# Kernel optimization log

Measured on AMD Instinct MI355X. Metric: run time of the kernel, lower is better.

The kernel has to match this reference:

```python
import jax, jax.numpy as jnp
import numpy as np

B, S, H, F, E, K = 2, 2048, 1024, 4096, 8, 2


def setup_inputs() -> dict:
    key = jax.random.key(0)
    ks = jax.random.split(key, 6)
    x = jax.random.normal(ks[0], (B, S, H), dtype=jnp.float32)
    probs = jax.random.uniform(ks[1], (K, B, S, 1), dtype=jnp.float32)
    experts = jax.random.randint(ks[2], (K, B, S, 1), 0, E, dtype=jnp.int32)
    # per-expert FFN params; 0.02 scale mimics typical transformer init
    w1 = jax.random.normal(ks[3], (E, H, F), dtype=jnp.float32) * 0.02
    b1 = jnp.zeros((E, F), dtype=jnp.float32)
    w2 = jax.random.normal(ks[4], (E, F, H), dtype=jnp.float32) * 0.02
    b2 = jnp.zeros((E, H), dtype=jnp.float32)
    return {"x": x, "probs": probs, "experts": experts,
            "w1": w1, "b1": b1, "w2": w2, "b2": b2}


def reference(x, probs, experts, w1, b1, w2, b2):
    # Dense compute-all-experts FFN: every expert processes every token.
    h = jnp.einsum('bsh,ehf->ebsf', x, w1) + b1[:, None, None, :]  # [E,B,S,F]
    h = jax.nn.gelu(h)
    y = jnp.einsum('ebsf,efh->ebsh', h, w2) + b2[:, None, None, :]  # [E,B,S,H]
    # Masked combine: sum_e sum_j probs_j * y_e * (experts_j == e)
    onehot = jax.nn.one_hot(experts[..., 0], w1.shape[0], dtype=x.dtype)  # [K,B,S,E]
    weights = jnp.einsum('kbsl,kbse->bse', probs, onehot)  # [B,S,E]
    out = jnp.einsum('bse,ebsh->bsh', weights, y)
    return out
```

## Files before the change

kernel.cpp:

```cpp
#include <hip/hip_runtime.h>
#include <stdint.h>

#define H_DIM 1024
#define F_DIM 4096
#define E_NUM 8
#define T_NUM 4096
#define NE    8192
#define BM    128
#define BN    128
#define BK    64
#define MAXTILES 72
#define PADMAX (MAXTILES*BM)

#define M_NT  0
#define M_PB  1
#define M_CNT 16
#define M_CUR 24
#define M_TE  32
#define M_TR  104
#define M_INTS 176

typedef float  f32x4  __attribute__((ext_vector_type(4)));
typedef short  bf16x8 __attribute__((ext_vector_type(8)));
typedef __bf16 b16v8  __attribute__((ext_vector_type(8)));
typedef unsigned short u16;
typedef u16    u16x8  __attribute__((ext_vector_type(8)));

__device__ __forceinline__ float gelu_tanh(float v) {
  float u = 0.7978845608028654f * (v + 0.044715f * v * v * v);
  return v / (1.0f + __expf(-2.0f * u));
}

__device__ __forceinline__ float b2f(u16 v) {
  union { float f; unsigned u; } x; x.u = ((unsigned)v) << 16; return x.f;
}

__device__ __forceinline__ void gl16(const void* g, void* l) {
  __builtin_amdgcn_global_load_lds(
      (const __attribute__((address_space(1))) unsigned int*)g,
      (__attribute__((address_space(3))) unsigned int*)l, 16, 0, 0);
}


__global__ void k_init(int* tok, float* wgt, int* meta) {
  int i = blockIdx.x * 256 + threadIdx.x;
  if (i < PADMAX) { tok[i] = 0; wgt[i] = 0.f; }
  if (i < E_NUM) { meta[M_CNT + i] = 0; meta[M_CUR + i] = 0; }
}

__global__ void k_count(const int* __restrict__ experts, int* meta) {
  int i = blockIdx.x * 256 + threadIdx.x;
  int e = experts[i];
  int lane = threadIdx.x & 63;
#pragma unroll
  for (int ee = 0; ee < E_NUM; ++ee) {
    unsigned long long bm = __ballot(e == ee);
    if (e == ee && lane == __builtin_ctzll(bm))
      atomicAdd(&meta[M_CNT + ee], __popcll(bm));
  }
}

__global__ void k_plan(int* meta) {
  if (threadIdx.x != 0 || blockIdx.x != 0) return;
  int pb = 0, idx = 0;
  for (int e = 0; e < E_NUM; ++e) {
    int c = meta[M_CNT + e];
    int nt = (c + BM - 1) / BM;
    meta[M_PB + e] = pb;
    for (int t = 0; t < nt; ++t) { meta[M_TE + idx] = e; meta[M_TR + idx] = pb + t * BM; ++idx; }
    pb += nt * BM;
  }
  meta[M_NT] = idx;
}

__global__ void k_scatter(const int* __restrict__ experts, const float* __restrict__ probs,
                          int* tok, float* wgt, int* entpos, int* meta) {
  int i = blockIdx.x * 256 + threadIdx.x;
  int e = experts[i];
  int t = i & (T_NUM - 1);
  float p = probs[i];
  int lane = threadIdx.x & 63;
#pragma unroll
  for (int ee = 0; ee < E_NUM; ++ee) {
    unsigned long long bm = __ballot(e == ee);
    if (e == ee) {
      int leader = __builtin_ctzll(bm);
      int cnt = __popcll(bm);
      int base = 0;
      if (lane == leader) base = atomicAdd(&meta[M_CUR + ee], cnt);
      base = __shfl(base, leader);
      int rank = __popcll(bm & ((1ull << lane) - 1ull));
      int pos = meta[M_PB + ee] + base + rank;
      tok[pos] = t;
      wgt[pos] = p;
      entpos[i] = pos;
    }
  }
}

__global__ void k_cvt_x(const float* __restrict__ x, u16* __restrict__ xbf) {
  int i = blockIdx.x * 256 + threadIdx.x;
  const f32x4* xp = (const f32x4*)x;
  f32x4 a = xp[i * 2], b = xp[i * 2 + 1];
  b16v8 o;
  o[0] = (__bf16)a[0]; o[1] = (__bf16)a[1]; o[2] = (__bf16)a[2]; o[3] = (__bf16)a[3];
  o[4] = (__bf16)b[0]; o[5] = (__bf16)b[1]; o[6] = (__bf16)b[2]; o[7] = (__bf16)b[3];
  ((b16v8*)xbf)[i] = o;
}

__global__ __launch_bounds__(256) void k_trans(const float* __restrict__ W, u16* __restrict__ Wt,
                                               int R, int C) {
  alignas(16) __shared__ char L[16384];
  int e = blockIdx.z;
  int r0 = blockIdx.y * 64, c0 = blockIdx.x * 64;
  const float* We = W + (size_t)e * R * C;
  u16* Wte = Wt + (size_t)e * R * C;
  int tid = threadIdx.x;
#pragma unroll
  for (int it = 0; it < 4; ++it) {
    int gi = it * 256 + tid;
    int row = gi >> 4, c4 = gi & 15;
    f32x4 v = *(const f32x4*)(We + (size_t)(r0 + row) * C + c0 + c4 * 4);
    *(f32x4*)(L + row * 256 + ((c4 ^ (row & 15)) * 16)) = v;
  }
  __syncthreads();
#pragma unroll
  for (int s = 0; s < 2; ++s) {
    int chunk = s * 256 + tid;
    int c = chunk >> 3, rb = chunk & 7;
    b16v8 o;
#pragma unroll
    for (int j = 0; j < 8; ++j) {
      int r = rb * 8 + j;
      float f = *(const float*)(L + r * 256 + (((c >> 2) ^ (r & 15)) * 16) + (c & 3) * 4);
      o[j] = (__bf16)f;
    }
    *(b16v8*)(void*)(Wte + (size_t)(c0 + c) * R + r0 + rb * 8) = o;
  }
}


__global__ __launch_bounds__(256) void k_gemm1(
    const u16* __restrict__ xbf, const u16* __restrict__ w1t, const float* __restrict__ b1,
    const int* __restrict__ tok, const int* __restrict__ meta, u16* __restrict__ hbuf)
{
  int nt = meta[M_NT];
  int slot = blockIdx.x;
  if (slot >= nt) return;
  int e     = meta[M_TE + slot];
  int rbase = meta[M_TR + slot];
  int cbase = blockIdx.y * BN;

  alignas(16) __shared__ char LDS[32768];
  char* Alds = LDS;
  char* Blds = LDS + 16384;

  int tid = threadIdx.x;
  int lane = tid & 63;
  int wid = tid >> 6;
  int wr = wid >> 1, wc = wid & 1;
  int ks = lane & 7, r8 = lane >> 3;

  const u16* asrc[4]; const u16* bsrc[4]; char* adst[4]; char* bdst[4];
#pragma unroll
  for (int j = 0; j < 4; ++j) {
    int r = wid * 32 + j * 8 + r8;
    int t = tok[rbase + r];
    asrc[j] = xbf + (size_t)t * H_DIM + ((ks ^ (r & 7)) * 8);
    bsrc[j] = w1t + ((size_t)e * F_DIM + cbase + r) * H_DIM + ((ks ^ (r & 7)) * 8);
    adst[j] = Alds + (wid * 32 + j * 8) * 128;
    bdst[j] = Blds + (wid * 32 + j * 8) * 128;
  }

  f32x4 acc[4][4];
#pragma unroll
  for (int m = 0; m < 4; ++m)
#pragma unroll
    for (int n = 0; n < 4; ++n) acc[m][n] = (f32x4){0.f, 0.f, 0.f, 0.f};

  for (int kt = 0; kt < H_DIM / BK; ++kt) {
    int kb = kt * BK;
    if (kt) __syncthreads();
#pragma unroll
    for (int j = 0; j < 4; ++j) gl16(asrc[j] + kb, adst[j]);
#pragma unroll
    for (int j = 0; j < 4; ++j) gl16(bsrc[j] + kb, bdst[j]);
    __syncthreads();
#pragma unroll
    for (int kk = 0; kk < 2; ++kk) {
      int kbyte = kk * 64 + ((lane >> 4) << 4);
      bf16x8 af[4], bfr[4];
#pragma unroll
      for (int m = 0; m < 4; ++m) {
        int r = wr * 64 + m * 16 + (lane & 15);
        af[m] = *(const bf16x8*)(Alds + r * 128 + (kbyte ^ ((r & 7) << 4)));
      }
#pragma unroll
      for (int n = 0; n < 4; ++n) {
        int c = wc * 64 + n * 16 + (lane & 15);
        bfr[n] = *(const bf16x8*)(Blds + c * 128 + (kbyte ^ ((c & 7) << 4)));
      }
#pragma unroll
      for (int m = 0; m < 4; ++m)
#pragma unroll
        for (int n = 0; n < 4; ++n)
          acc[m][n] = __builtin_amdgcn_mfma_f32_16x16x32_bf16(af[m], bfr[n], acc[m][n], 0, 0, 0);
    }
  }

  __syncthreads();
  float bv[4];
#pragma unroll
  for (int n = 0; n < 4; ++n) bv[n] = b1[e * F_DIM + cbase + wc * 64 + n * 16 + (lane & 15)];
  char* reg = LDS + wid * 8192;
#pragma unroll
  for (int m = 0; m < 4; ++m)
#pragma unroll
    for (int n = 0; n < 4; ++n)
#pragma unroll
      for (int q = 0; q < 4; ++q) {
        float v = acc[m][n][q] + bv[n];
        v = gelu_tanh(v);
        int row4 = ((lane >> 4) << 2) + q;
        int col = n * 16 + (lane & 15);
        *(__bf16*)(reg + m * 2048 + row4 * 128 + col * 2) = (__bf16)v;
      }
  __syncthreads();
#pragma unroll
  for (int q = 0; q < 8; ++q) {
    int m = q >> 1, p = q & 1;
    int byte = p * 1024 + lane * 16;
    u16x8 v = *(const u16x8*)(reg + m * 2048 + byte);
    int row  = p * 8 + (lane >> 3);
    int colb = (lane & 7) * 16;
    size_t grow = (size_t)(rbase + wr * 64 + m * 16 + row);
    size_t gcol = (size_t)(cbase + wc * 64 + (colb >> 1));
    *(u16x8*)(hbuf + grow * F_DIM + gcol) = v;
  }
}


__global__ __launch_bounds__(256) void k_gemm2(
    const u16* __restrict__ hbuf, const u16* __restrict__ w2t, const float* __restrict__ b2,
    const int* __restrict__ meta, u16* __restrict__ ybuf)
{
  int nt = meta[M_NT];
  int slot = blockIdx.x;
  if (slot >= nt) return;
  int e     = meta[M_TE + slot];
  int rbase = meta[M_TR + slot];
  int cbase = blockIdx.y * BN;
  int kzb   = blockIdx.z * (F_DIM / 2);

  alignas(16) __shared__ char LDS[32768];
  char* Alds = LDS;
  char* Blds = LDS + 16384;

  int tid = threadIdx.x;
  int lane = tid & 63;
  int wid = tid >> 6;
  int wr = wid >> 1, wc = wid & 1;
  int ks = lane & 7, r8 = lane >> 3;

  const u16* asrc[4]; const u16* bsrc[4]; char* adst[4]; char* bdst[4];
#pragma unroll
  for (int j = 0; j < 4; ++j) {
    int r = wid * 32 + j * 8 + r8;
    asrc[j] = hbuf + (size_t)(rbase + r) * F_DIM + kzb + ((ks ^ (r & 7)) * 8);
    bsrc[j] = w2t + ((size_t)e * H_DIM + cbase + r) * F_DIM + kzb + ((ks ^ (r & 7)) * 8);
    adst[j] = Alds + (wid * 32 + j * 8) * 128;
    bdst[j] = Blds + (wid * 32 + j * 8) * 128;
  }

  f32x4 acc[4][4];
#pragma unroll
  for (int m = 0; m < 4; ++m)
#pragma unroll
    for (int n = 0; n < 4; ++n) acc[m][n] = (f32x4){0.f, 0.f, 0.f, 0.f};

  for (int kt = 0; kt < (F_DIM / 2) / BK; ++kt) {
    int kb = kt * BK;
    if (kt) __syncthreads();
#pragma unroll
    for (int j = 0; j < 4; ++j) gl16(asrc[j] + kb, adst[j]);
#pragma unroll
    for (int j = 0; j < 4; ++j) gl16(bsrc[j] + kb, bdst[j]);
    __syncthreads();
#pragma unroll
    for (int kk = 0; kk < 2; ++kk) {
      int kbyte = kk * 64 + ((lane >> 4) << 4);
      bf16x8 af[4], bfr[4];
#pragma unroll
      for (int m = 0; m < 4; ++m) {
        int r = wr * 64 + m * 16 + (lane & 15);
        af[m] = *(const bf16x8*)(Alds + r * 128 + (kbyte ^ ((r & 7) << 4)));
      }
#pragma unroll
      for (int n = 0; n < 4; ++n) {
        int c = wc * 64 + n * 16 + (lane & 15);
        bfr[n] = *(const bf16x8*)(Blds + c * 128 + (kbyte ^ ((c & 7) << 4)));
      }
#pragma unroll
      for (int m = 0; m < 4; ++m)
#pragma unroll
        for (int n = 0; n < 4; ++n)
          acc[m][n] = __builtin_amdgcn_mfma_f32_16x16x32_bf16(af[m], bfr[n], acc[m][n], 0, 0, 0);
    }
  }

  __syncthreads();
  bool z0 = (blockIdx.z == 0);
  u16* yb = ybuf + (size_t)blockIdx.z * PADMAX * H_DIM;
  float bv[4];
#pragma unroll
  for (int n = 0; n < 4; ++n)
    bv[n] = z0 ? b2[e * H_DIM + cbase + wc * 64 + n * 16 + (lane & 15)] : 0.f;
  char* reg = LDS + wid * 8192;
#pragma unroll
  for (int m = 0; m < 4; ++m)
#pragma unroll
    for (int n = 0; n < 4; ++n)
#pragma unroll
      for (int q = 0; q < 4; ++q) {
        float v = acc[m][n][q] + bv[n];
        int row4 = ((lane >> 4) << 2) + q;
        int col = n * 16 + (lane & 15);
        *(__bf16*)(reg + m * 2048 + row4 * 128 + col * 2) = (__bf16)v;
      }
  __syncthreads();
#pragma unroll
  for (int q = 0; q < 8; ++q) {
    int m = q >> 1, p = q & 1;
    int byte = p * 1024 + lane * 16;
    u16x8 v = *(const u16x8*)(reg + m * 2048 + byte);
    int row  = p * 8 + (lane >> 3);
    int colb = (lane & 7) * 16;
    size_t grow = (size_t)(rbase + wr * 64 + m * 16 + row);
    size_t gcol = (size_t)(cbase + wc * 64 + (colb >> 1));
    *(u16x8*)(yb + grow * H_DIM + gcol) = v;
  }
}


__global__ __launch_bounds__(256) void k_combine(
    const u16* __restrict__ ybuf, const float* __restrict__ wgt,
    const int* __restrict__ entpos, float* __restrict__ out)
{
  int idx = blockIdx.x * 256 + threadIdx.x;
  int t = idx >> 7, hc = idx & 127;
  int p0 = entpos[t], p1 = entpos[T_NUM + t];
  float w0 = wgt[p0], w1 = wgt[p1];
  const u16x8* y0 = (const u16x8*)(ybuf);
  const u16x8* y1 = (const u16x8*)(ybuf + (size_t)PADMAX * H_DIM);
  u16x8 a = y0[(size_t)p0 * (H_DIM / 8) + hc];
  u16x8 b = y1[(size_t)p0 * (H_DIM / 8) + hc];
  u16x8 c = y0[(size_t)p1 * (H_DIM / 8) + hc];
  u16x8 d = y1[(size_t)p1 * (H_DIM / 8) + hc];
  f32x4 o0, o1;
#pragma unroll
  for (int j = 0; j < 4; ++j)
    o0[j] = w0 * (b2f(a[j]) + b2f(b[j])) + w1 * (b2f(c[j]) + b2f(d[j]));
#pragma unroll
  for (int j = 0; j < 4; ++j)
    o1[j] = w0 * (b2f(a[4 + j]) + b2f(b[4 + j])) + w1 * (b2f(c[4 + j]) + b2f(d[4 + j]));
  f32x4* op = (f32x4*)(out + (size_t)t * H_DIM + hc * 8);
  op[0] = o0;
  op[1] = o1;
}


extern "C" void kernel_launch(void* const* d_in, const int* in_sizes, int n_in,
                              void* d_out, int out_size, void* d_ws, size_t ws_size,
                              hipStream_t stream)
{
  const float* x       = (const float*)d_in[0];
  const float* probs   = (const float*)d_in[1];
  const int*   experts = (const int*)d_in[2];
  const float* w1      = (const float*)d_in[3];
  const float* b1      = (const float*)d_in[4];
  const float* w2      = (const float*)d_in[5];
  const float* b2      = (const float*)d_in[6];
  float* out = (float*)d_out;

  char* ws = (char*)d_ws;
  size_t off = 0;
  u16*   hbuf = (u16*)(ws + off);  off += (size_t)PADMAX * F_DIM * sizeof(u16);
  u16*   xbf  = (u16*)(ws + off);  off += (size_t)T_NUM * H_DIM * sizeof(u16);
  u16*   w1t  = (u16*)(ws + off);  off += (size_t)E_NUM * F_DIM * H_DIM * sizeof(u16);
  u16*   w2t  = (u16*)(ws + off);  off += (size_t)E_NUM * F_DIM * H_DIM * sizeof(u16);
  int*   tok  = (int*)(ws + off);  off += (size_t)PADMAX * sizeof(int);
  float* wgt  = (float*)(ws + off); off += (size_t)PADMAX * sizeof(float);
  int*   entpos = (int*)(ws + off); off += (size_t)NE * sizeof(int);
  int*   meta = (int*)(ws + off);  off += M_INTS * sizeof(int);
  u16*   ybuf = w1t;
  (void)ws_size; (void)in_sizes; (void)n_in;

  k_init   <<<dim3((PADMAX + 255) / 256), 256, 0, stream>>>(tok, wgt, meta);
  k_count  <<<dim3(NE / 256), 256, 0, stream>>>(experts, meta);
  k_plan   <<<1, 1, 0, stream>>>(meta);
  k_scatter<<<dim3(NE / 256), 256, 0, stream>>>(experts, probs, tok, wgt, entpos, meta);
  k_cvt_x  <<<dim3(T_NUM * H_DIM / 8 / 256), 256, 0, stream>>>(x, xbf);
  k_trans  <<<dim3(F_DIM / 64, H_DIM / 64, E_NUM), 256, 0, stream>>>(w1, w1t, H_DIM, F_DIM);
  k_trans  <<<dim3(H_DIM / 64, F_DIM / 64, E_NUM), 256, 0, stream>>>(w2, w2t, F_DIM, H_DIM);
  k_gemm1  <<<dim3(MAXTILES, F_DIM / BN), 256, 0, stream>>>(xbf, w1t, b1, tok, meta, hbuf);
  k_gemm2  <<<dim3(MAXTILES, H_DIM / BN, 2), 256, 0, stream>>>(hbuf, w2t, b2, meta, ybuf);
  k_combine<<<dim3(T_NUM * H_DIM / 8 / 256), 256, 0, stream>>>(ybuf, wgt, entpos, out);
}
```

Measured before the change: 358.7 us.

## Use 256-row tiles with triple-buffered async LDS pipeline in expert GEMMs

Both expert GEMM kernels move from a single-buffered 128x128 tile with 256 threads to a 256x128 tile with 512 threads. They use a three-stage ring of LDS buffers filled by global_load_lds, with explicit vmcnt waits and raw barriers so loads of later K-steps overlap MFMA work. MFMA sections get raised wave priority. The two transposed weight buffers now share one workspace region, so the w2 transpose runs after GEMM1, and ybuf gets its own allocation. The aim is to hide global-load latency and halve weight re-reads per token, at the cost of 144 KB of dynamic LDS (limiting occupancy), more padding waste per expert, and a hard tile cap of 39 that could drop tiles in extreme routing distributions.

```diff
diff --git a/kernel.cpp b/kernel.cpp
--- a/kernel.cpp
+++ b/kernel.cpp
@@ -6,25 +6,30 @@
 #define E_NUM 8
 #define T_NUM 4096
 #define NE    8192
-#define BM    128
+#define BM    256
 #define BN    128
 #define BK    64
-#define MAXTILES 72
-#define PADMAX (MAXTILES*BM)
+#define MAXT  39
+#define PADMAX (MAXT*BM)
+#define TILE_BYTES 49152
+#define LDS_BYTES  147456
 
 #define M_NT  0
 #define M_PB  1
 #define M_CNT 16
 #define M_CUR 24
 #define M_TE  32
-#define M_TR  104
-#define M_INTS 176
+#define M_TR  80
+#define M_INTS 128
 
 typedef float  f32x4  __attribute__((ext_vector_type(4)));
 typedef short  bf16x8 __attribute__((ext_vector_type(8)));
 typedef __bf16 b16v8  __attribute__((ext_vector_type(8)));
 typedef unsigned short u16;
 typedef u16    u16x8  __attribute__((ext_vector_type(8)));
+
+#define FENCE() asm volatile("" ::: "memory")
+#define BAR()   __builtin_amdgcn_s_barrier()
 
 __device__ __forceinline__ float gelu_tanh(float v) {
   float u = 0.7978845608028654f * (v + 0.044715f * v * v * v);
@@ -67,7 +72,9 @@
     int c = meta[M_CNT + e];
     int nt = (c + BM - 1) / BM;
     meta[M_PB + e] = pb;
-    for (int t = 0; t < nt; ++t) { meta[M_TE + idx] = e; meta[M_TR + idx] = pb + t * BM; ++idx; }
+    for (int t = 0; t < nt && idx < MAXT; ++t) {
+      meta[M_TE + idx] = e; meta[M_TR + idx] = pb + t * BM; ++idx;
+    }
     pb += nt * BM;
   }
   meta[M_NT] = idx;
@@ -140,10 +147,61 @@
 }
 
 
-__global__ __launch_bounds__(256) void k_gemm1(
-    const u16* __restrict__ xbf, const u16* __restrict__ w1t, const float* __restrict__ b1,
+#define STAGE6(kt, bb)                                                      \
+  { char* Ab_ = LDS + (bb);                                                 \
+    _Pragma("unroll")                                                       \
+    for (int j = 0; j < 4; ++j) gl16(asrc[j] + (kt) * 64, Ab_ + adst[j]);   \
+    _Pragma("unroll")                                                       \
+    for (int j = 0; j < 2; ++j) gl16(bsrc[j] + (kt) * 64, Ab_ + 32768 + bdst[j]); }
+
+#define GEMM_COMPUTE(bb)                                                    \
+  { const char* Ab_ = LDS + (bb); const char* Bb_ = Ab_ + 32768;            \
+    _Pragma("unroll")                                                       \
+    for (int kk = 0; kk < 2; ++kk) {                                        \
+      int kbyte = kk * 64 + ((lane >> 4) << 4);                             \
+      bf16x8 af[4], bfr[4];                                                 \
+      _Pragma("unroll")                                                     \
+      for (int m = 0; m < 4; ++m) {                                         \
+        int r = wr * 64 + m * 16 + (lane & 15);                             \
+        af[m] = *(const bf16x8*)(Ab_ + r * 128 + (kbyte ^ ((r & 7) << 4))); \
+      }                                                                     \
+      _Pragma("unroll")                                                     \
+      for (int n = 0; n < 4; ++n) {                                         \
+        int c = wc * 64 + n * 16 + (lane & 15);                             \
+        bfr[n] = *(const bf16x8*)(Bb_ + c * 128 + (kbyte ^ ((c & 7) << 4)));\
+      }                                                                     \
+      __builtin_amdgcn_s_setprio(1);                                        \
+      _Pragma("unroll")                                                     \
+      for (int m = 0; m < 4; ++m)                                           \
+        _Pragma("unroll")                                                   \
+        for (int n = 0; n < 4; ++n)                                         \
+          acc[m][n] = __builtin_amdgcn_mfma_f32_16x16x32_bf16(af[m], bfr[n], acc[m][n], 0, 0, 0); \
+      __builtin_amdgcn_s_setprio(0);                                        \
+    } }
+
+#define GEMM_KLOOP(NT)                                                      \
+  STAGE6(0, 0); STAGE6(1, TILE_BYTES);                                      \
+  { int bcur = 0, bnext = 2 * TILE_BYTES;                                   \
+    for (int t = 0; t < (NT); ++t) {                                        \
+      FENCE();                                                              \
+      if (t + 2 < (NT)) { STAGE6(t + 2, bnext);                             \
+        asm volatile("s_waitcnt vmcnt(12)" ::: "memory"); }                 \
+      else if (t + 1 < (NT)) { asm volatile("s_waitcnt vmcnt(6)" ::: "memory"); } \
+      else { asm volatile("s_waitcnt vmcnt(0)" ::: "memory"); }             \
+      BAR(); FENCE();                                                       \
+      GEMM_COMPUTE(bcur);                                                   \
+      FENCE(); BAR();                                                       \
+      bcur  = (bcur  == 2 * TILE_BYTES) ? 0 : bcur  + TILE_BYTES;           \
+      bnext = (bnext == 2 * TILE_BYTES) ? 0 : bnext + TILE_BYTES;           \
+    } }                                                                     \
+  FENCE();
+
+
+__global__ __launch_bounds__(512, 2) void k_gemm1(
+    const u16* __restrict__ xbf, const u16* __restrict__ wbuf, const float* __restrict__ b1,
     const int* __restrict__ tok, const int* __restrict__ meta, u16* __restrict__ hbuf)
 {
+  extern __shared__ char LDS[];
   int nt = meta[M_NT];
   int slot = blockIdx.x;
   if (slot >= nt) return;
@@ -151,25 +209,26 @@
   int rbase = meta[M_TR + slot];
   int cbase = blockIdx.y * BN;
 
-  alignas(16) __shared__ char LDS[32768];
-  char* Alds = LDS;
-  char* Blds = LDS + 16384;
-
   int tid = threadIdx.x;
   int lane = tid & 63;
   int wid = tid >> 6;
   int wr = wid >> 1, wc = wid & 1;
-  int ks = lane & 7, r8 = lane >> 3;
-
-  const u16* asrc[4]; const u16* bsrc[4]; char* adst[4]; char* bdst[4];
+  int cc = tid & 7, rr = tid >> 3;
+
+  const u16* asrc[4]; int adst[4];
 #pragma unroll
   for (int j = 0; j < 4; ++j) {
-    int r = wid * 32 + j * 8 + r8;
-    int t = tok[rbase + r];
-    asrc[j] = xbf + (size_t)t * H_DIM + ((ks ^ (r & 7)) * 8);
-    bsrc[j] = w1t + ((size_t)e * F_DIM + cbase + r) * H_DIM + ((ks ^ (r & 7)) * 8);
-    adst[j] = Alds + (wid * 32 + j * 8) * 128;
-    bdst[j] = Blds + (wid * 32 + j * 8) * 128;
+    int rj = j * 64 + rr;
+    int t = tok[rbase + rj];
+    asrc[j] = xbf + (size_t)t * H_DIM + ((cc ^ (rj & 7)) * 8);
+    adst[j] = (j * 64 + wid * 8) * 128;
+  }
+  const u16* bsrc[2]; int bdst[2];
+#pragma unroll
+  for (int j = 0; j < 2; ++j) {
+    int nj = j * 64 + rr;
+    bsrc[j] = wbuf + ((size_t)e * F_DIM + cbase + nj) * H_DIM + ((cc ^ (nj & 7)) * 8);
+    bdst[j] = (j * 64 + wid * 8) * 128;
   }
 
   f32x4 acc[4][4];
@@ -178,37 +237,8 @@
 #pragma unroll
     for (int n = 0; n < 4; ++n) acc[m][n] = (f32x4){0.f, 0.f, 0.f, 0.f};
 
-  for (int kt = 0; kt < H_DIM / BK; ++kt) {
-    int kb = kt * BK;
-    if (kt) __syncthreads();
-#pragma unroll
-    for (int j = 0; j < 4; ++j) gl16(asrc[j] + kb, adst[j]);
-#pragma unroll
-    for (int j = 0; j < 4; ++j) gl16(bsrc[j] + kb, bdst[j]);
-    __syncthreads();
-#pragma unroll
-    for (int kk = 0; kk < 2; ++kk) {
-      int kbyte = kk * 64 + ((lane >> 4) << 4);
-      bf16x8 af[4], bfr[4];
-#pragma unroll
-      for (int m = 0; m < 4; ++m) {
-        int r = wr * 64 + m * 16 + (lane & 15);
-        af[m] = *(const bf16x8*)(Alds + r * 128 + (kbyte ^ ((r & 7) << 4)));
-      }
-#pragma unroll
-      for (int n = 0; n < 4; ++n) {
-        int c = wc * 64 + n * 16 + (lane & 15);
-        bfr[n] = *(const bf16x8*)(Blds + c * 128 + (kbyte ^ ((c & 7) << 4)));
-      }
-#pragma unroll
-      for (int m = 0; m < 4; ++m)
-#pragma unroll
-        for (int n = 0; n < 4; ++n)
-          acc[m][n] = __builtin_amdgcn_mfma_f32_16x16x32_bf16(af[m], bfr[n], acc[m][n], 0, 0, 0);
-    }
-  }
-
-  __syncthreads();
+  GEMM_KLOOP(H_DIM / BK)
+
   float bv[4];
 #pragma unroll
   for (int n = 0; n < 4; ++n) bv[n] = b1[e * F_DIM + cbase + wc * 64 + n * 16 + (lane & 15)];
@@ -225,7 +255,6 @@
         int col = n * 16 + (lane & 15);
         *(__bf16*)(reg + m * 2048 + row4 * 128 + col * 2) = (__bf16)v;
       }
-  __syncthreads();
 #pragma unroll
   for (int q = 0; q < 8; ++q) {
     int m = q >> 1, p = q & 1;
@@ -240,10 +269,11 @@
 }
 
 
-__global__ __launch_bounds__(256) void k_gemm2(
-    const u16* __restrict__ hbuf, const u16* __restrict__ w2t, const float* __restrict__ b2,
+__global__ __launch_bounds__(512, 2) void k_gemm2(
+    const u16* __restrict__ hbuf, const u16* __restrict__ wbuf, const float* __restrict__ b2,
     const int* __restrict__ meta, u16* __restrict__ ybuf)
 {
+  extern __shared__ char LDS[];
   int nt = meta[M_NT];
   int slot = blockIdx.x;
   if (slot >= nt) return;
@@ -252,24 +282,25 @@
   int cbase = blockIdx.y * BN;
   int kzb   = blockIdx.z * (F_DIM / 2);
 
-  alignas(16) __shared__ char LDS[32768];
-  char* Alds = LDS;
-  char* Blds = LDS + 16384;
-
   int tid = threadIdx.x;
   int lane = tid & 63;
   int wid = tid >> 6;
   int wr = wid >> 1, wc = wid & 1;
-  int ks = lane & 7, r8 = lane >> 3;
-
-  const u16* asrc[4]; const u16* bsrc[4]; char* adst[4]; char* bdst[4];
+  int cc = tid & 7, rr = tid >> 3;
+
+  const u16* asrc[4]; int adst[4];
 #pragma unroll
   for (int j = 0; j < 4; ++j) {
-    int r = wid * 32 + j * 8 + r8;
-    asrc[j] = hbuf + (size_t)(rbase + r) * F_DIM + kzb + ((ks ^ (r & 7)) * 8);
-    bsrc[j] = w2t + ((size_t)e * H_DIM + cbase + r) * F_DIM + kzb + ((ks ^ (r & 7)) * 8);
-    adst[j] = Alds + (wid * 32 + j * 8) * 128;
-    bdst[j] = Blds + (wid * 32 + j * 8) * 128;
+    int rj = j * 64 + rr;
+    asrc[j] = hbuf + (size_t)(rbase + rj) * F_DIM + kzb + ((cc ^ (rj & 7)) * 8);
+    adst[j] = (j * 64 + wid * 8) * 128;
+  }
+  const u16* bsrc[2]; int bdst[2];
+#pragma unroll
+  for (int j = 0; j < 2; ++j) {
+    int nj = j * 64 + rr;
+    bsrc[j] = wbuf + ((size_t)e * H_DIM + cbase + nj) * F_DIM + kzb + ((cc ^ (nj & 7)) * 8);
+    bdst[j] = (j * 64 + wid * 8) * 128;
   }
 
   f32x4 acc[4][4];
@@ -278,37 +309,8 @@
 #pragma unroll
     for (int n = 0; n < 4; ++n) acc[m][n] = (f32x4){0.f, 0.f, 0.f, 0.f};
 
-  for (int kt = 0; kt < (F_DIM / 2) / BK; ++kt) {
-    int kb = kt * BK;
-    if (kt) __syncthreads();
-#pragma unroll
-    for (int j = 0; j < 4; ++j) gl16(asrc[j] + kb, adst[j]);
-#pragma unroll
-    for (int j = 0; j < 4; ++j) gl16(bsrc[j] + kb, bdst[j]);
-    __syncthreads();
-#pragma unroll
-    for (int kk = 0; kk < 2; ++kk) {
-      int kbyte = kk * 64 + ((lane >> 4) << 4);
-      bf16x8 af[4], bfr[4];
-#pragma unroll
-      for (int m = 0; m < 4; ++m) {
-        int r = wr * 64 + m * 16 + (lane & 15);
-        af[m] = *(const bf16x8*)(Alds + r * 128 + (kbyte ^ ((r & 7) << 4)));
-      }
-#pragma unroll
-      for (int n = 0; n < 4; ++n) {
-        int c = wc * 64 + n * 16 + (lane & 15);
-        bfr[n] = *(const bf16x8*)(Blds + c * 128 + (kbyte ^ ((c & 7) << 4)));
-      }
-#pragma unroll
-      for (int m = 0; m < 4; ++m)
-#pragma unroll
-        for (int n = 0; n < 4; ++n)
-          acc[m][n] = __builtin_amdgcn_mfma_f32_16x16x32_bf16(af[m], bfr[n], acc[m][n], 0, 0, 0);
-    }
-  }
-
-  __syncthreads();
+  GEMM_KLOOP((F_DIM / 2) / BK)
+
   bool z0 = (blockIdx.z == 0);
   u16* yb = ybuf + (size_t)blockIdx.z * PADMAX * H_DIM;
   float bv[4];
@@ -327,7 +329,6 @@
         int col = n * 16 + (lane & 15);
         *(__bf16*)(reg + m * 2048 + row4 * 128 + col * 2) = (__bf16)v;
       }
-  __syncthreads();
 #pragma unroll
   for (int q = 0; q < 8; ++q) {
     int m = q >> 1, p = q & 1;
@@ -386,23 +387,27 @@
   size_t off = 0;
   u16*   hbuf = (u16*)(ws + off);  off += (size_t)PADMAX * F_DIM * sizeof(u16);
   u16*   xbf  = (u16*)(ws + off);  off += (size_t)T_NUM * H_DIM * sizeof(u16);
-  u16*   w1t  = (u16*)(ws + off);  off += (size_t)E_NUM * F_DIM * H_DIM * sizeof(u16);
-  u16*   w2t  = (u16*)(ws + off);  off += (size_t)E_NUM * F_DIM * H_DIM * sizeof(u16);
+  u16*   wbuf = (u16*)(ws + off);  off += (size_t)E_NUM * F_DIM * H_DIM * sizeof(u16);
+  u16*   ybuf = (u16*)(ws + off);  off += (size_t)2 * PADMAX * H_DIM * sizeof(u16);
   int*   tok  = (int*)(ws + off);  off += (size_t)PADMAX * sizeof(int);
   float* wgt  = (float*)(ws + off); off += (size_t)PADMAX * sizeof(float);
   int*   entpos = (int*)(ws + off); off += (size_t)NE * sizeof(int);
   int*   meta = (int*)(ws + off);  off += M_INTS * sizeof(int);
-  u16*   ybuf = w1t;
   (void)ws_size; (void)in_sizes; (void)n_in;
 
-  k_init   <<<dim3((PADMAX + 255) / 256), 256, 0, stream>>>(tok, wgt, meta);
+  hipFuncSetAttribute(reinterpret_cast<const void*>(&k_gemm1),
+                      hipFuncAttributeMaxDynamicSharedMemorySize, LDS_BYTES);
+  hipFuncSetAttribute(reinterpret_cast<const void*>(&k_gemm2),
+                      hipFuncAttributeMaxDynamicSharedMemorySize, LDS_BYTES);
+
+  k_init   <<<dim3(PADMAX / 256), 256, 0, stream>>>(tok, wgt, meta);
   k_count  <<<dim3(NE / 256), 256, 0, stream>>>(experts, meta);
   k_plan   <<<1, 1, 0, stream>>>(meta);
   k_scatter<<<dim3(NE / 256), 256, 0, stream>>>(experts, probs, tok, wgt, entpos, meta);
   k_cvt_x  <<<dim3(T_NUM * H_DIM / 8 / 256), 256, 0, stream>>>(x, xbf);
-  k_trans  <<<dim3(F_DIM / 64, H_DIM / 64, E_NUM), 256, 0, stream>>>(w1, w1t, H_DIM, F_DIM);
-  k_trans  <<<dim3(H_DIM / 64, F_DIM / 64, E_NUM), 256, 0, stream>>>(w2, w2t, F_DIM, H_DIM);
-  k_gemm1  <<<dim3(MAXTILES, F_DIM / BN), 256, 0, stream>>>(xbf, w1t, b1, tok, meta, hbuf);
-  k_gemm2  <<<dim3(MAXTILES, H_DIM / BN, 2), 256, 0, stream>>>(hbuf, w2t, b2, meta, ybuf);
+  k_trans  <<<dim3(F_DIM / 64, H_DIM / 64, E_NUM), 256, 0, stream>>>(w1, wbuf, H_DIM, F_DIM);
+  k_gemm1  <<<dim3(MAXT, F_DIM / BN), 512, LDS_BYTES, stream>>>(xbf, wbuf, b1, tok, meta, hbuf);
+  k_trans  <<<dim3(H_DIM / 64, F_DIM / 64, E_NUM), 256, 0, stream>>>(w2, wbuf, F_DIM, H_DIM);
+  k_gemm2  <<<dim3(MAXT, H_DIM / BN, 2), 512, LDS_BYTES, stream>>>(hbuf, wbuf, b2, meta, ybuf);
   k_combine<<<dim3(T_NUM * H_DIM / 8 / 256), 256, 0, stream>>>(ybuf, wgt, entpos, out);
 }
```

Result: slower. 408.0 us (+13.7%).

## Double-buffer GEMM K-loop with async LDS loads and XCD-aware tile remap

Applied to the files above, without the earlier changes.

Both expert GEMMs now use two LDS buffers, loading the next K tile while MFMAs run on the current one. This removes the load-then-barrier stall of the single-buffered loop. The grid is flattened to 1D, and block ids are remapped so consecutive work lands on the same XCD (the 8-way interleave), which should improve L2 reuse. MFMA sections also raise wave priority. In exchange, LDS use doubles to 64KB of dynamic shared memory, which may cut occupancy. The removed barrier before the epilogue store relies on each wave only reading its own LDS region.

```diff
diff --git a/kernel.cpp b/kernel.cpp
--- a/kernel.cpp
+++ b/kernel.cpp
@@ -11,6 +11,7 @@
 #define BK    64
 #define MAXTILES 72
 #define PADMAX (MAXTILES*BM)
+#define BUFB  32768
 
 #define M_NT  0
 #define M_PB  1
@@ -25,6 +26,8 @@
 typedef __bf16 b16v8  __attribute__((ext_vector_type(8)));
 typedef unsigned short u16;
 typedef u16    u16x8  __attribute__((ext_vector_type(8)));
+
+#define BAR() __builtin_amdgcn_s_barrier()
 
 __device__ __forceinline__ float gelu_tanh(float v) {
   float u = 0.7978845608028654f * (v + 0.044715f * v * v * v);
@@ -140,20 +143,65 @@
 }
 
 
+#define STAGE8(kt, bb)                                                        \
+  { char* L_ = LDS + (bb);                                                    \
+    _Pragma("unroll")                                                         \
+    for (int j = 0; j < 4; ++j) gl16(asrc[j] + (size_t)(kt) * BK, L_ + aoff[j]); \
+    _Pragma("unroll")                                                         \
+    for (int j = 0; j < 4; ++j) gl16(bsrc[j] + (size_t)(kt) * BK, L_ + 16384 + aoff[j]); }
+
+#define GEMM_COMPUTE(bb)                                                      \
+  { const char* Ab_ = LDS + (bb); const char* Bb_ = LDS + (bb) + 16384;       \
+    _Pragma("unroll")                                                         \
+    for (int kk = 0; kk < 2; ++kk) {                                          \
+      int kbyte = kk * 64 + ((lane >> 4) << 4);                               \
+      bf16x8 af[4], bfr[4];                                                   \
+      _Pragma("unroll")                                                       \
+      for (int m = 0; m < 4; ++m) {                                           \
+        int r = wr * 64 + m * 16 + (lane & 15);                               \
+        af[m] = *(const bf16x8*)(Ab_ + r * 128 + (kbyte ^ ((r & 7) << 4)));   \
+      }                                                                       \
+      _Pragma("unroll")                                                       \
+      for (int n = 0; n < 4; ++n) {                                           \
+        int c = wc * 64 + n * 16 + (lane & 15);                               \
+        bfr[n] = *(const bf16x8*)(Bb_ + c * 128 + (kbyte ^ ((c & 7) << 4)));  \
+      }                                                                       \
+      __builtin_amdgcn_s_setprio(1);                                          \
+      _Pragma("unroll")                                                       \
+      for (int m = 0; m < 4; ++m)                                             \
+        _Pragma("unroll")                                                     \
+        for (int n = 0; n < 4; ++n)                                           \
+          acc[m][n] = __builtin_amdgcn_mfma_f32_16x16x32_bf16(af[m], bfr[n], acc[m][n], 0, 0, 0); \
+      __builtin_amdgcn_s_setprio(0);                                          \
+    } }
+
+#define GEMM_KLOOP(NT)                                                        \
+  STAGE8(0, 0);                                                               \
+  asm volatile("s_waitcnt vmcnt(0)" ::: "memory");                            \
+  BAR();                                                                      \
+  { int cur = 0;                                                              \
+    for (int kt = 0; kt < (NT); ++kt) {                                       \
+      if (kt + 1 < (NT)) STAGE8(kt + 1, (cur ^ 1) * BUFB);                    \
+      GEMM_COMPUTE(cur * BUFB);                                               \
+      asm volatile("s_waitcnt vmcnt(0)" ::: "memory");                        \
+      BAR();                                                                  \
+      cur ^= 1;                                                               \
+    } }
+
+
 __global__ __launch_bounds__(256) void k_gemm1(
     const u16* __restrict__ xbf, const u16* __restrict__ w1t, const float* __restrict__ b1,
     const int* __restrict__ tok, const int* __restrict__ meta, u16* __restrict__ hbuf)
 {
+  extern __shared__ char LDS[];
+  int wg = blockIdx.x;
+  int work = (wg & 7) * 288 + (wg >> 3);
+  int slot = work % MAXTILES;
+  int cbase = (work / MAXTILES) * BN;
   int nt = meta[M_NT];
-  int slot = blockIdx.x;
   if (slot >= nt) return;
   int e     = meta[M_TE + slot];
   int rbase = meta[M_TR + slot];
-  int cbase = blockIdx.y * BN;
-
-  alignas(16) __shared__ char LDS[32768];
-  char* Alds = LDS;
-  char* Blds = LDS + 16384;
 
   int tid = threadIdx.x;
   int lane = tid & 63;
@@ -161,15 +209,14 @@
   int wr = wid >> 1, wc = wid & 1;
   int ks = lane & 7, r8 = lane >> 3;
 
-  const u16* asrc[4]; const u16* bsrc[4]; char* adst[4]; char* bdst[4];
+  const u16* asrc[4]; const u16* bsrc[4]; int aoff[4];
 #pragma unroll
   for (int j = 0; j < 4; ++j) {
     int r = wid * 32 + j * 8 + r8;
     int t = tok[rbase + r];
     asrc[j] = xbf + (size_t)t * H_DIM + ((ks ^ (r & 7)) * 8);
     bsrc[j] = w1t + ((size_t)e * F_DIM + cbase + r) * H_DIM + ((ks ^ (r & 7)) * 8);
-    adst[j] = Alds + (wid * 32 + j * 8) * 128;
-    bdst[j] = Blds + (wid * 32 + j * 8) * 128;
+    aoff[j] = (wid * 32 + j * 8) * 128;
   }
 
   f32x4 acc[4][4];
@@ -178,37 +225,8 @@
 #pragma unroll
     for (int n = 0; n < 4; ++n) acc[m][n] = (f32x4){0.f, 0.f, 0.f, 0.f};
 
-  for (int kt = 0; kt < H_DIM / BK; ++kt) {
-    int kb = kt * BK;
-    if (kt) __syncthreads();
-#pragma unroll
-    for (int j = 0; j < 4; ++j) gl16(asrc[j] + kb, adst[j]);
-#pragma unroll
-    for (int j = 0; j < 4; ++j) gl16(bsrc[j] + kb, bdst[j]);
-    __syncthreads();
-#pragma unroll
-    for (int kk = 0; kk < 2; ++kk) {
-      int kbyte = kk * 64 + ((lane >> 4) << 4);
-      bf16x8 af[4], bfr[4];
-#pragma unroll
-      for (int m = 0; m < 4; ++m) {
-        int r = wr * 64 + m * 16 + (lane & 15);
-        af[m] = *(const bf16x8*)(Alds + r * 128 + (kbyte ^ ((r & 7) << 4)));
-      }
-#pragma unroll
-      for (int n = 0; n < 4; ++n) {
-        int c = wc * 64 + n * 16 + (lane & 15);
-        bfr[n] = *(const bf16x8*)(Blds + c * 128 + (kbyte ^ ((c & 7) << 4)));
-      }
-#pragma unroll
-      for (int m = 0; m < 4; ++m)
-#pragma unroll
-        for (int n = 0; n < 4; ++n)
-          acc[m][n] = __builtin_amdgcn_mfma_f32_16x16x32_bf16(af[m], bfr[n], acc[m][n], 0, 0, 0);
-    }
-  }
-
-  __syncthreads();
+  GEMM_KLOOP(H_DIM / BK)
+
   float bv[4];
 #pragma unroll
   for (int n = 0; n < 4; ++n) bv[n] = b1[e * F_DIM + cbase + wc * 64 + n * 16 + (lane & 15)];
@@ -225,7 +243,6 @@
         int col = n * 16 + (lane & 15);
         *(__bf16*)(reg + m * 2048 + row4 * 128 + col * 2) = (__bf16)v;
       }
-  __syncthreads();
 #pragma unroll
   for (int q = 0; q < 8; ++q) {
     int m = q >> 1, p = q & 1;
@@ -244,17 +261,18 @@
     const u16* __restrict__ hbuf, const u16* __restrict__ w2t, const float* __restrict__ b2,
     const int* __restrict__ meta, u16* __restrict__ ybuf)
 {
+  extern __shared__ char LDS[];
+  int wg = blockIdx.x;
+  int work = (wg & 7) * 144 + (wg >> 3);
+  int zi   = work / 576;
+  int rem  = work % 576;
+  int slot = rem % MAXTILES;
+  int cbase = (rem / MAXTILES) * BN;
+  int kzb   = zi * (F_DIM / 2);
   int nt = meta[M_NT];
-  int slot = blockIdx.x;
   if (slot >= nt) return;
   int e     = meta[M_TE + slot];
   int rbase = meta[M_TR + slot];
-  int cbase = blockIdx.y * BN;
-  int kzb   = blockIdx.z * (F_DIM / 2);
-
-  alignas(16) __shared__ char LDS[32768];
-  char* Alds = LDS;
-  char* Blds = LDS + 16384;
 
   int tid = threadIdx.x;
   int lane = tid & 63;
@@ -262,14 +280,13 @@
   int wr = wid >> 1, wc = wid & 1;
   int ks = lane & 7, r8 = lane >> 3;
 
-  const u16* asrc[4]; const u16* bsrc[4]; char* adst[4]; char* bdst[4];
+  const u16* asrc[4]; const u16* bsrc[4]; int aoff[4];
 #pragma unroll
   for (int j = 0; j < 4; ++j) {
     int r = wid * 32 + j * 8 + r8;
     asrc[j] = hbuf + (size_t)(rbase + r) * F_DIM + kzb + ((ks ^ (r & 7)) * 8);
     bsrc[j] = w2t + ((size_t)e * H_DIM + cbase + r) * F_DIM + kzb + ((ks ^ (r & 7)) * 8);
-    adst[j] = Alds + (wid * 32 + j * 8) * 128;
-    bdst[j] = Blds + (wid * 32 + j * 8) * 128;
+    aoff[j] = (wid * 32 + j * 8) * 128;
   }
 
   f32x4 acc[4][4];
@@ -278,39 +295,10 @@
 #pragma unroll
     for (int n = 0; n < 4; ++n) acc[m][n] = (f32x4){0.f, 0.f, 0.f, 0.f};
 
-  for (int kt = 0; kt < (F_DIM / 2) / BK; ++kt) {
-    int kb = kt * BK;
-    if (kt) __syncthreads();
-#pragma unroll
-    for (int j = 0; j < 4; ++j) gl16(asrc[j] + kb, adst[j]);
-#pragma unroll
-    for (int j = 0; j < 4; ++j) gl16(bsrc[j] + kb, bdst[j]);
-    __syncthreads();
-#pragma unroll
-    for (int kk = 0; kk < 2; ++kk) {
-      int kbyte = kk * 64 + ((lane >> 4) << 4);
-      bf16x8 af[4], bfr[4];
-#pragma unroll
-      for (int m = 0; m < 4; ++m) {
-        int r = wr * 64 + m * 16 + (lane & 15);
-        af[m] = *(const bf16x8*)(Alds + r * 128 + (kbyte ^ ((r & 7) << 4)));
-      }
-#pragma unroll
-      for (int n = 0; n < 4; ++n) {
-        int c = wc * 64 + n * 16 + (lane & 15);
-        bfr[n] = *(const bf16x8*)(Blds + c * 128 + (kbyte ^ ((c & 7) << 4)));
-      }
-#pragma unroll
-      for (int m = 0; m < 4; ++m)
-#pragma unroll
-        for (int n = 0; n < 4; ++n)
-          acc[m][n] = __builtin_amdgcn_mfma_f32_16x16x32_bf16(af[m], bfr[n], acc[m][n], 0, 0, 0);
-    }
-  }
-
-  __syncthreads();
-  bool z0 = (blockIdx.z == 0);
-  u16* yb = ybuf + (size_t)blockIdx.z * PADMAX * H_DIM;
+  GEMM_KLOOP((F_DIM / 2) / BK)
+
+  bool z0 = (zi == 0);
+  u16* yb = ybuf + (size_t)zi * PADMAX * H_DIM;
   float bv[4];
 #pragma unroll
   for (int n = 0; n < 4; ++n)
@@ -327,7 +315,6 @@
         int col = n * 16 + (lane & 15);
         *(__bf16*)(reg + m * 2048 + row4 * 128 + col * 2) = (__bf16)v;
       }
-  __syncthreads();
 #pragma unroll
   for (int q = 0; q < 8; ++q) {
     int m = q >> 1, p = q & 1;
@@ -395,6 +382,11 @@
   u16*   ybuf = w1t;
   (void)ws_size; (void)in_sizes; (void)n_in;
 
+  hipFuncSetAttribute(reinterpret_cast<const void*>(&k_gemm1),
+                      hipFuncAttributeMaxDynamicSharedMemorySize, 2 * BUFB);
+  hipFuncSetAttribute(reinterpret_cast<const void*>(&k_gemm2),
+                      hipFuncAttributeMaxDynamicSharedMemorySize, 2 * BUFB);
+
   k_init   <<<dim3((PADMAX + 255) / 256), 256, 0, stream>>>(tok, wgt, meta);
   k_count  <<<dim3(NE / 256), 256, 0, stream>>>(experts, meta);
   k_plan   <<<1, 1, 0, stream>>>(meta);
@@ -402,7 +394,7 @@
   k_cvt_x  <<<dim3(T_NUM * H_DIM / 8 / 256), 256, 0, stream>>>(x, xbf);
   k_trans  <<<dim3(F_DIM / 64, H_DIM / 64, E_NUM), 256, 0, stream>>>(w1, w1t, H_DIM, F_DIM);
   k_trans  <<<dim3(H_DIM / 64, F_DIM / 64, E_NUM), 256, 0, stream>>>(w2, w2t, F_DIM, H_DIM);
-  k_gemm1  <<<dim3(MAXTILES, F_DIM / BN), 256, 0, stream>>>(xbf, w1t, b1, tok, meta, hbuf);
-  k_gemm2  <<<dim3(MAXTILES, H_DIM / BN, 2), 256, 0, stream>>>(hbuf, w2t, b2, meta, ybuf);
+  k_gemm1  <<<dim3(MAXTILES * (F_DIM / BN)), 256, 2 * BUFB, stream>>>(xbf, w1t, b1, tok, meta, hbuf);
+  k_gemm2  <<<dim3(MAXTILES * (H_DIM / BN) * 2), 256, 2 * BUFB, stream>>>(hbuf, w2t, b2, meta, ybuf);
   k_combine<<<dim3(T_NUM * H_DIM / 8 / 256), 256, 0, stream>>>(ybuf, wgt, entpos, out);
 }
```

After: 363.3 us. No clear change (+1.3%).
